# Kernel optimization log

Hardware: AMD Instinct MI355X
Metric: run time of the kernel (lower is better)

## Reference

```python
import jax, jax.numpy as jnp
import numpy as np

B, S, D, E, H, K = 2, 2048, 1024, 8, 2048, 2
EM_ITERS = 5
LB_WEIGHT = 0.1
EPS = 1e-8


def setup_inputs() -> dict:
    key = jax.random.key(0)
    ks = jax.random.split(key, 12)
    sc = 0.02
    return {
        "x": jax.random.normal(ks[0], (B, S, D), jnp.float32),
        "gate_W": jax.random.normal(ks[1], (D, E), jnp.float32) * sc,
        "gate_b": jnp.zeros((E,), jnp.float32),
        "gate_temp": jnp.ones((1,), jnp.float32),
        "W1": jax.random.normal(ks[2], (E, D, H), jnp.float32) * sc,
        "b1": jnp.zeros((E, H), jnp.float32),
        "W2": jax.random.normal(ks[3], (E, H, D), jnp.float32) * sc,
        "b2": jnp.zeros((E, D), jnp.float32),
        "sW1": jax.random.normal(ks[4], (D, H), jnp.float32) * sc,
        "sb1": jnp.zeros((H,), jnp.float32),
        "sW2": jax.random.normal(ks[5], (H, D), jnp.float32) * sc,
        "sb2": jnp.zeros((D,), jnp.float32),
    }


def reference(x, gate_W, gate_b, gate_temp, W1, b1, W2, b2, sW1, sb1, sW2, sb2):
    Bq, Sq, Dq = x.shape
    T = Bq * Sq
    xf = x.reshape(T, Dq)  # (T, D)

    # Router: gate linear + learned temperature
    gate_logits = xf @ gate_W + gate_b              # (T, E)
    tempered = gate_logits / gate_temp               # (T, E)
    expert_weights = jax.nn.softmax(tempered, axis=-1)
    _, topk_idx = jax.lax.top_k(expert_weights, K)   # (T, K) int32
    first = topk_idx[:, 0]

    # Load-balance loss: KL(uniform || empirical top-1 usage) (fresh counters)
    usage = jnp.zeros((E,), jnp.float32).at[first].add(1.0)
    actual = usage / jnp.float32(T)
    actual = actual + EPS
    actual = actual / actual.sum()
    u = jnp.float32(1.0 / E)
    kl = jnp.sum(u * (jnp.log(u) - jnp.log(actual)))
    load_balance_loss = LB_WEIGHT * kl

    # EM expert-load reweighting on tempered logits
    scores = jax.nn.softmax(tempered, axis=-1)       # (T, E)
    p = jnp.full((E,), 1.0 / E, jnp.float32)
    for _ in range(EM_ITERS):
        ea = scores * p                               # (T, E)
        ea = ea / (ea.sum(axis=-1, keepdims=True) + EPS)
        counts = ea.sum(axis=0)                       # (E,)
        p = counts / (counts.sum() + EPS)
    balanced = scores * p                             # (T, E)

    # All-expert FFN (dense, equivalent to per-expert masked compute)
    h = jax.nn.relu(jnp.einsum('td,edh->teh', xf, W1) + b1)  # (T, E, H)
    eo = jnp.einsum('teh,ehd->ted', h, W2) + b2              # (T, E, D)

    # Combine top-k experts with balanced weights
    w_k = jnp.take_along_axis(balanced, topk_idx, axis=1)        # (T, K)
    out_k = jnp.take_along_axis(eo, topk_idx[:, :, None], axis=1)  # (T, K, D)
    out = jnp.einsum('tk,tkd->td', w_k, out_k)                   # (T, D)

    # Shared expert, weighted by 0.1
    shared = jax.nn.relu(xf @ sW1 + sb1) @ sW2 + sb2
    out = out + 0.1 * shared

    return out.reshape(Bq, Sq, Dq), load_balance_loss
```

## Files before the change

### kernel.cpp

```cpp
#include <hip/hip_runtime.h>
#include <math.h>

#define T_TOK 4096
#define D_DIM 1024
#define H_DIM 2048
#define NE 8
#define EPSF 1e-8f
#define G1_GEMM 896
#define G2_GEMM 448
#define NTR128 1152

typedef __attribute__((ext_vector_type(8))) short bf16x8;
typedef __attribute__((ext_vector_type(4))) float f32x4;

__device__ __forceinline__ unsigned short f2bf(float f) {
  unsigned u = __float_as_uint(f);
  u += 0x7fffu + ((u >> 16) & 1u);
  return (unsigned short)(u >> 16);
}

__device__ __forceinline__ void gload_lds16(const void* g, void* l) {
  __builtin_amdgcn_global_load_lds(
      (const __attribute__((address_space(1))) unsigned int*)g,
      (__attribute__((address_space(3))) unsigned int*)l, 16, 0, 0);
}

#define WAITV(n) asm volatile("s_waitcnt vmcnt(" #n ")" ::: "memory")
#define BARR()                                  \
  do {                                          \
    asm volatile("" ::: "memory");              \
    __builtin_amdgcn_s_barrier();               \
    asm volatile("" ::: "memory");              \
  } while (0)

__device__ __forceinline__ void transpose_tile128(const float* __restrict__ src,
                                                  unsigned short* __restrict__ dst,
                                                  int R, int C, int r0, int c0, int tid,
                                                  float* tile) {
#pragma unroll
  for (int k = 0; k < 8; ++k) {
    int id = tid + k * 512;
    int row = id >> 5, c4 = (id & 31) * 4;
    float4 v = *(const float4*)(src + (size_t)(r0 + row) * C + c0 + c4);
    float* tr = tile + row * 129 + c4;
    tr[0] = v.x; tr[1] = v.y; tr[2] = v.z; tr[3] = v.w;
  }
  __syncthreads();
#pragma unroll
  for (int k = 0; k < 4; ++k) {
    int id = tid + k * 512;
    int oc = id >> 4;
    int rbase = (id & 15) * 8;
    uint4 wv;
    unsigned* wp = (unsigned*)&wv;
#pragma unroll
    for (int j = 0; j < 4; ++j) {
      unsigned lo = f2bf(tile[(rbase + 2 * j) * 129 + oc]);
      unsigned hi = f2bf(tile[(rbase + 2 * j + 1) * 129 + oc]);
      wp[j] = lo | (hi << 16);
    }
    *(uint4*)(dst + (size_t)(c0 + oc) * R + r0 + rbase) = wv;
  }
}

__global__ __launch_bounds__(512, 4) void prep2_kernel(
    const float* __restrict__ x, const float* __restrict__ gW, const float* __restrict__ gb,
    const float* __restrict__ gtemp, const float* __restrict__ W1, const float* __restrict__ sW1,
    unsigned short* __restrict__ W1t, unsigned short* __restrict__ sW1t,
    unsigned short* __restrict__ xb, float* __restrict__ scores, int* __restrict__ idx,
    unsigned* __restrict__ usage, unsigned* __restrict__ cnt, int* __restrict__ perm) {
  __shared__ char psm[67584];
  int b = blockIdx.x, tid = threadIdx.x;
  if (b >= 512) {
    int l = b - 512;
    int m = l >> 7, rem = l & 127;
    int c0 = (rem & 15) * 128, r0 = (rem >> 4) * 128;
    const float* src = (m < NE) ? W1 + (size_t)m * D_DIM * H_DIM : sW1;
    unsigned short* dst = (m < NE) ? W1t + (size_t)m * D_DIM * H_DIM : sW1t;
    transpose_tile128(src, dst, D_DIM, H_DIM, r0, c0, tid, (float*)psm);
    return;
  }
  float* gWl = (float*)psm;
  int* toks = (int*)(psm + 36864);
  int wave = tid >> 6, lane = tid & 63;
  int t0 = b * 8;
#pragma unroll
  for (int k = 0; k < 4; ++k) {
    int q = tid + k * 512;
    float4 f = ((const float4*)gW)[q];
    int d = q >> 1, eo = (q & 1) * 4;
    float* dstv = &gWl[d * 9 + eo];
    dstv[0] = f.x; dstv[1] = f.y; dstv[2] = f.z; dstv[3] = f.w;
  }
  __syncthreads();
  int t = t0 + wave;
  const float* xr = x + (size_t)t * D_DIM;
  unsigned short* xbr = xb + (size_t)t * D_DIM;
  float part[NE];
#pragma unroll
  for (int e = 0; e < NE; ++e) part[e] = 0.f;
#pragma unroll
  for (int i = 0; i < 16; ++i) {
    int d = lane + 64 * i;
    float xv = xr[d];
    xbr[d] = f2bf(xv);
    const float* g = &gWl[d * 9];
#pragma unroll
    for (int e = 0; e < NE; ++e) part[e] += xv * g[e];
  }
#pragma unroll
  for (int e = 0; e < NE; ++e) {
    float v = part[e];
    for (int off = 32; off; off >>= 1) v += __shfl_xor(v, off);
    part[e] = v;
  }
  float temp = gtemp[0];
  float mx = -1e30f;
#pragma unroll
  for (int e = 0; e < NE; ++e) { part[e] = (part[e] + gb[e]) / temp; mx = fmaxf(mx, part[e]); }
  float s = 0.f;
#pragma unroll
  for (int e = 0; e < NE; ++e) { part[e] = expf(part[e] - mx); s += part[e]; }
  float inv = 1.0f / s;
#pragma unroll
  for (int e = 0; e < NE; ++e) part[e] *= inv;
  if (lane == 0) {
    float4* sp = (float4*)(scores + (size_t)t * NE);
    sp[0] = make_float4(part[0], part[1], part[2], part[3]);
    sp[1] = make_float4(part[4], part[5], part[6], part[7]);
    int i0 = 0; float b0 = part[0];
#pragma unroll
    for (int e = 1; e < NE; ++e) if (part[e] > b0) { b0 = part[e]; i0 = e; }
    int i1 = -1; float b1 = -1e30f;
#pragma unroll
    for (int e = 0; e < NE; ++e) if (e != i0 && part[e] > b1) { b1 = part[e]; i1 = e; }
    idx[t * 2] = i0; idx[t * 2 + 1] = i1;
    toks[wave * 2] = i0; toks[wave * 2 + 1] = i1;
  }
  __syncthreads();
  if (tid < NE) {
    int c0 = 0, c1 = 0;
#pragma unroll
    for (int j = 0; j < 8; ++j) {
      if (toks[j * 2] == tid) ++c0;
      if (toks[j * 2 + 1] == tid) ++c1;
    }
    if (c0) atomicAdd(&usage[tid], (unsigned)c0);
    int tot = c0 + c1;
    if (tot) {
      unsigned bb = atomicAdd(&cnt[tid], (unsigned)tot);
      int p = 0;
#pragma unroll
      for (int j = 0; j < 8; ++j) {
        if (toks[j * 2] == tid) perm[(size_t)tid * T_TOK + bb + p++] = (t0 + j) * 2;
        if (toks[j * 2 + 1] == tid) perm[(size_t)tid * T_TOK + bb + p++] = (t0 + j) * 2 + 1;
      }
    }
  }
}

__device__ __forceinline__ void em_block512(const float* __restrict__ scores,
                                            const unsigned* __restrict__ usage,
                                            float* __restrict__ p_out, float* __restrict__ loss_out,
                                            int tid, char* smem) {
  float* p_sh = (float*)smem;
  float* cw = p_sh + 8;
  float* counts_sh = cw + 64;
  int wave = tid >> 6, lane = tid & 63;
  float s[8][NE];
#pragma unroll
  for (int rr = 0; rr < 8; ++rr) {
    int row = tid + rr * 512;
    const float4* sp = (const float4*)(scores + (size_t)row * NE);
    float4 a = sp[0], b = sp[1];
    s[rr][0] = a.x; s[rr][1] = a.y; s[rr][2] = a.z; s[rr][3] = a.w;
    s[rr][4] = b.x; s[rr][5] = b.y; s[rr][6] = b.z; s[rr][7] = b.w;
  }
  if (tid < NE) p_sh[tid] = 1.0f / NE;
  __syncthreads();
  for (int it = 0; it < 5; ++it) {
    float p[NE];
#pragma unroll
    for (int e = 0; e < NE; ++e) p[e] = p_sh[e];
    float c[NE];
#pragma unroll
    for (int e = 0; e < NE; ++e) c[e] = 0.f;
#pragma unroll
    for (int rr = 0; rr < 8; ++rr) {
      float denom = 0.f;
#pragma unroll
      for (int e = 0; e < NE; ++e) denom += s[rr][e] * p[e];
      float inv = 1.0f / (denom + EPSF);
#pragma unroll
      for (int e = 0; e < NE; ++e) c[e] += s[rr][e] * p[e] * inv;
    }
#pragma unroll
    for (int e = 0; e < NE; ++e) {
      float v = c[e];
      for (int off = 32; off; off >>= 1) v += __shfl_xor(v, off);
      c[e] = v;
    }
    if (lane == 0) {
#pragma unroll
      for (int e = 0; e < NE; ++e) cw[wave * 8 + e] = c[e];
    }
    __syncthreads();
    if (tid < NE) {
      float tot = 0.f;
#pragma unroll
      for (int w = 0; w < 8; ++w) tot += cw[w * 8 + tid];
      counts_sh[tid] = tot;
    }
    __syncthreads();
    if (tid < NE) {
      float total = 0.f;
#pragma unroll
      for (int e = 0; e < NE; ++e) total += counts_sh[e];
      p_sh[tid] = counts_sh[tid] / (total + EPSF);
    }
    __syncthreads();
  }
  if (tid < NE) p_out[tid] = p_sh[tid];
  if (tid == 0) {
    float actual[NE]; float norm = 0.f;
#pragma unroll
    for (int e = 0; e < NE; ++e) { actual[e] = (float)usage[e] / (float)T_TOK + EPSF; norm += actual[e]; }
    float u = 1.0f / NE;
    float kl = 0.f;
#pragma unroll
    for (int e = 0; e < NE; ++e) kl += u * (logf(u) - logf(actual[e] / norm));
    loss_out[0] = 0.1f * kl;
  }
}

template <int KDIM, int NDIM, bool RELU, bool MODE1>
__device__ __forceinline__ void gemm_body(
    unsigned short* lds, int flat,
    const unsigned short* __restrict__ A, const unsigned short* __restrict__ WE,
    const unsigned short* __restrict__ WS, const float* __restrict__ biasE,
    const float* __restrict__ biasS, const int* __restrict__ perm,
    const unsigned* __restrict__ cnt, void* __restrict__ outp) {
  constexpr int BM = 256, BN = 128, BK = 32;
  constexpr int NT = NDIM / BN;
  constexpr int NKT = KDIM / BK;

  int tc[9];
#pragma unroll
  for (int i = 0; i < NE; ++i) tc[i] = ((int)cnt[i] + 255) >> 8;
  tc[8] = T_TOK / 256;
  int nt = 0;
#pragma unroll
  for (int i = 0; i < 9; ++i) nt += tc[i];
  int W = nt * NT;
  int xcd = flat & 7, pos = flat >> 3;
  int q = W >> 3, r = W & 7;
  int mycount = q + (xcd < r ? 1 : 0);
  if (pos >= mycount) return;
  int mystart = xcd * q + (xcd < r ? xcd : r);
  int w = mystart + pos;
  int ti = w / NT;
  int n0 = (w % NT) * BN;
  int e = 0, mt = ti;
  while (mt >= tc[e]) { mt -= tc[e]; ++e; }
  int m0 = mt * BM;
  int cnt_e = (e == NE) ? T_TOK : (int)cnt[e];

  const unsigned short* Bmat = (e == NE) ? WS : WE + (size_t)e * KDIM * NDIM;
  const float* bias = (e == NE) ? biasS : biasE + (size_t)e * NDIM;

  int tid = threadIdx.x, wave = tid >> 6, lane = tid & 63;
  int wm = wave >> 1, wn = wave & 1;
  int frow = lane & 15, fks = lane >> 4;

  auto garf = [&](int rrow) {
    int ar = m0 + rrow; if (ar > cnt_e - 1) ar = cnt_e - 1;
    int gar;
    if (e == NE) gar = MODE1 ? ar : (2 * T_TOK + ar);
    else { int v = perm[(size_t)e * T_TOK + ar]; gar = MODE1 ? (v >> 1) : v; }
    return gar;
  };
  int r0a = wave * 16 + (lane >> 2);
  int r1a = 128 + wave * 16 + (lane >> 2);
  int rb = wave * 16 + (lane >> 2);
  int g0 = (r0a & 3) ^ ((r0a >> 2) & 3);
  int g1 = (r1a & 3) ^ ((r1a >> 2) & 3);
  int gbv = (rb & 3) ^ ((rb >> 2) & 3);
  const unsigned short* aptr0 = A + (size_t)garf(r0a) * KDIM + (((lane & 3) ^ g0) << 3);
  const unsigned short* aptr1 = A + (size_t)garf(r1a) * KDIM + (((lane & 3) ^ g1) << 3);
  const unsigned short* bptr = Bmat + (size_t)(n0 + rb) * KDIM + (((lane & 3) ^ gbv) << 3);

  auto stA = [&](int t, int ab) {
    gload_lds16(aptr0 + t * BK, &lds[ab * 8192 + wave * 512]);
    gload_lds16(aptr1 + t * BK, &lds[ab * 8192 + 4096 + wave * 512]);
  };
  auto stB = [&](int t) {
    gload_lds16(bptr + t * BK, &lds[24576 + (t & 1) * 4096 + wave * 512]);
  };

  auto rdA = [&](int ab, int m) -> bf16x8 {
    int rr = wm * 64 + m * 16 + frow;
    int sp = fks ^ ((rr & 3) ^ ((rr >> 2) & 3));
    return *(const bf16x8*)&lds[ab * 8192 + rr * 32 + sp * 8];
  };
  auto rdB = [&](int bb, int j) -> bf16x8 {
    int rr = wn * 64 + j * 16 + frow;
    int sp = fks ^ ((rr & 3) ^ ((rr >> 2) & 3));
    return *(const bf16x8*)&lds[24576 + bb * 4096 + rr * 32 + sp * 8];
  };

  f32x4 acc[4][4];
#pragma unroll
  for (int m = 0; m < 4; ++m)
#pragma unroll
    for (int j = 0; j < 4; ++j) acc[m][j] = (f32x4){0.f, 0.f, 0.f, 0.f};

  stA(0, 0); stB(0); stA(1, 1);
  WAITV(2);
  BARR();

  int ab = 0;
  for (int t = 0; t < NKT; ++t) {
    int bb = t & 1;
    bf16x8 a[4], b[4];
#pragma unroll
    for (int m = 0; m < 4; ++m) a[m] = rdA(ab, m);
#pragma unroll
    for (int j = 0; j < 4; ++j) b[j] = rdB(bb, j);
    if (t + 1 < NKT) stB(t + 1);
    if (t + 2 < NKT) { int ab2 = ab + 2; if (ab2 >= 3) ab2 -= 3; stA(t + 2, ab2); }
    BARR();
    __builtin_amdgcn_s_setprio(1);
#pragma unroll
    for (int m = 0; m < 4; ++m)
#pragma unroll
      for (int j = 0; j < 4; ++j)
        acc[m][j] = __builtin_amdgcn_mfma_f32_16x16x32_bf16(a[m], b[j], acc[m][j], 0, 0, 0);
    __builtin_amdgcn_s_setprio(0);
    if (t + 1 < NKT) {
      if (t + 2 < NKT) { WAITV(2); } else { WAITV(0); }
      BARR();
    }
    ab = (ab == 2) ? 0 : ab + 1;
  }

#pragma unroll
  for (int m = 0; m < 4; ++m) {
#pragma unroll
    for (int qq = 0; qq < 4; ++qq) {
      int rt = wm * 64 + m * 16 + (lane >> 4) * 4 + qq;
      if (m0 + rt >= cnt_e) continue;
      int rr;
      if (e == NE) rr = 2 * T_TOK + m0 + rt;
      else rr = perm[(size_t)e * T_TOK + m0 + rt];
#pragma unroll
      for (int j = 0; j < 4; ++j) {
        int col = n0 + wn * 64 + j * 16 + (lane & 15);
        float val = acc[m][j][qq] + bias[col];
        if (RELU) val = fmaxf(val, 0.f);
        if (MODE1)
          ((unsigned short*)outp)[(size_t)rr * NDIM + col] = f2bf(val);
        else
          ((float*)outp)[(size_t)rr * NDIM + col] = val;
      }
    }
  }
}

__global__ __launch_bounds__(512, 4) void gemm1_kernel(
    const unsigned short* __restrict__ xb, const unsigned short* __restrict__ W1t,
    const unsigned short* __restrict__ sW1t, const float* __restrict__ b1,
    const float* __restrict__ sb1, const int* __restrict__ perm, const unsigned* __restrict__ cnt,
    unsigned short* __restrict__ Hbuf,
    const float* __restrict__ W2, const float* __restrict__ sW2,
    unsigned short* __restrict__ W2t, unsigned short* __restrict__ sW2t,
    const float* __restrict__ scores, const unsigned* __restrict__ usage,
    float* __restrict__ pbuf, float* __restrict__ loss_out) {
  __shared__ char smem[67584];
  int flat = blockIdx.x;
  if (flat < G1_GEMM) {
    gemm_body<D_DIM, H_DIM, true, true>((unsigned short*)smem, flat, xb, W1t, sW1t, b1, sb1,
                                        perm, cnt, (void*)Hbuf);
    return;
  }
  int l = flat - G1_GEMM;
  if (l < NTR128) {
    int m = l >> 7, rem = l & 127;
    int c0 = (rem & 7) * 128, r0 = (rem >> 3) * 128;
    const float* src = (m < NE) ? W2 + (size_t)m * H_DIM * D_DIM : sW2;
    unsigned short* dst = (m < NE) ? W2t + (size_t)m * H_DIM * D_DIM : sW2t;
    transpose_tile128(src, dst, H_DIM, D_DIM, r0, c0, threadIdx.x, (float*)smem);
    return;
  }
  em_block512(scores, usage, pbuf, loss_out, threadIdx.x, smem);
}

template <int KDIM, int NDIM, bool RELU, bool MODE1>
__global__ __launch_bounds__(512, 4) void gemm_kernel(
    const unsigned short* __restrict__ A, const unsigned short* __restrict__ WE,
    const unsigned short* __restrict__ WS, const float* __restrict__ biasE,
    const float* __restrict__ biasS, const int* __restrict__ perm,
    const unsigned* __restrict__ cnt, void* __restrict__ outp) {
  __shared__ char smem[67584];
  gemm_body<KDIM, NDIM, RELU, MODE1>((unsigned short*)smem, blockIdx.x, A, WE, WS, biasE, biasS,
                                     perm, cnt, outp);
}

__global__ void combine_kernel(const float* __restrict__ ebuf, const float* __restrict__ scores,
                               const float* __restrict__ p, const int* __restrict__ idx,
                               float* __restrict__ out) {
  int gid = blockIdx.x * blockDim.x + threadIdx.x;
  int t = gid >> 8;
  int d4 = gid & 255;
  int e0 = idx[t * 2], e1 = idx[t * 2 + 1];
  float w0 = scores[(size_t)t * NE + e0] * p[e0];
  float w1 = scores[(size_t)t * NE + e1] * p[e1];
  const float4* r0 = (const float4*)(ebuf + (size_t)(t * 2) * D_DIM);
  const float4* r1 = (const float4*)(ebuf + (size_t)(t * 2 + 1) * D_DIM);
  const float4* rs = (const float4*)(ebuf + (size_t)(2 * T_TOK + t) * D_DIM);
  float4 a = r0[d4], b = r1[d4], c = rs[d4];
  float4 o;
  o.x = w0 * a.x + w1 * b.x + 0.1f * c.x;
  o.y = w0 * a.y + w1 * b.y + 0.1f * c.y;
  o.z = w0 * a.z + w1 * b.z + 0.1f * c.z;
  o.w = w0 * a.w + w1 * b.w + 0.1f * c.w;
  ((float4*)out)[gid] = o;
}

extern "C" void kernel_launch(void* const* d_in, const int* in_sizes, int n_in,
                              void* d_out, int out_size, void* d_ws, size_t ws_size,
                              hipStream_t stream) {
  const float* x     = (const float*)d_in[0];
  const float* gW    = (const float*)d_in[1];
  const float* gb    = (const float*)d_in[2];
  const float* gtemp = (const float*)d_in[3];
  const float* W1    = (const float*)d_in[4];
  const float* b1    = (const float*)d_in[5];
  const float* W2    = (const float*)d_in[6];
  const float* b2    = (const float*)d_in[7];
  const float* sW1   = (const float*)d_in[8];
  const float* sb1   = (const float*)d_in[9];
  const float* sW2   = (const float*)d_in[10];
  const float* sb2   = (const float*)d_in[11];
  float* out = (float*)d_out;

  char* ws = (char*)d_ws;
  size_t off = 0;
  auto take = [&](size_t b) { char* ptr = ws + off; off += (b + 255) & ~(size_t)255; return ptr; };
  unsigned short* xb   = (unsigned short*)take((size_t)T_TOK * D_DIM * 2);
  unsigned short* W1t  = (unsigned short*)take((size_t)NE * H_DIM * D_DIM * 2);
  unsigned short* sW1t = (unsigned short*)take((size_t)H_DIM * D_DIM * 2);
  unsigned short* W2t  = (unsigned short*)take((size_t)NE * D_DIM * H_DIM * 2);
  unsigned short* sW2t = (unsigned short*)take((size_t)D_DIM * H_DIM * 2);
  unsigned short* Hbuf = (unsigned short*)take((size_t)3 * T_TOK * H_DIM * 2);
  float* ebuf          = (float*)take((size_t)3 * T_TOK * D_DIM * 4);
  float* scores        = (float*)take((size_t)T_TOK * NE * 4);
  int* idx             = (int*)take((size_t)T_TOK * 2 * 4);
  int* perm            = (int*)take((size_t)NE * T_TOK * 4);
  unsigned* cnt        = (unsigned*)take(256);
  unsigned* usage      = (unsigned*)take(256);
  float* pbuf          = (float*)take(256);
  (void)n_in; (void)in_sizes; (void)out_size; (void)ws_size;

  hipMemsetAsync(cnt, 0, 512, stream);
  prep2_kernel<<<512 + NTR128, 512, 0, stream>>>(x, gW, gb, gtemp, W1, sW1, W1t, sW1t, xb,
                                                 scores, idx, usage, cnt, perm);
  gemm1_kernel<<<G1_GEMM + NTR128 + 1, 512, 0, stream>>>(
      xb, W1t, sW1t, b1, sb1, perm, cnt, Hbuf, W2, sW2, W2t, sW2t, scores, usage, pbuf,
      out + (size_t)T_TOK * D_DIM);
  gemm_kernel<H_DIM, D_DIM, false, false><<<G2_GEMM, 512, 0, stream>>>(
      Hbuf, W2t, sW2t, b2, sb2, perm, cnt, (void*)ebuf);
  combine_kernel<<<(T_TOK * D_DIM / 4) / 256, 256, 0, stream>>>(ebuf, scores, pbuf, idx, out);
}
```

Measured before the change: 203.5 us.

## Retile grouped GEMM to 128x256x64 with triple-buffered B and larger LDS

Changes the grouped expert GEMM tile from 256x128 with BK=32 to 128x256 with BK=64. A is now double-buffered and B triple-buffered, using a new XOR swizzle on 64-element rows, and each iteration issues two MFMA k-steps. LDS grows to 128KB, so launch bounds drop to one block per CU. The grid sizes are recomputed for the new tile counts. The aim is fewer barriers per unit of work and better reuse of the per-expert weight tiles. In exchange, occupancy drops and padding waste on small per-expert token counts rises with the finer M granularity.

```diff
diff --git a/kernel.cpp b/kernel.cpp
--- a/kernel.cpp
+++ b/kernel.cpp
@@ -6,8 +6,8 @@
 #define H_DIM 2048
 #define NE 8
 #define EPSF 1e-8f
-#define G1_GEMM 896
-#define G2_GEMM 448
+#define G1_GEMM 832
+#define G2_GEMM 416
 #define NTR128 1152
 
 typedef __attribute__((ext_vector_type(8))) short bf16x8;
@@ -26,6 +26,7 @@
 }
 
 #define WAITV(n) asm volatile("s_waitcnt vmcnt(" #n ")" ::: "memory")
+#define WAITL() asm volatile("s_waitcnt lgkmcnt(0)" ::: "memory")
 #define BARR()                                  \
   do {                                          \
     asm volatile("" ::: "memory");              \
@@ -240,14 +241,14 @@
     const unsigned short* __restrict__ WS, const float* __restrict__ biasE,
     const float* __restrict__ biasS, const int* __restrict__ perm,
     const unsigned* __restrict__ cnt, void* __restrict__ outp) {
-  constexpr int BM = 256, BN = 128, BK = 32;
+  constexpr int BM = 128, BN = 256, BK = 64;
   constexpr int NT = NDIM / BN;
   constexpr int NKT = KDIM / BK;
 
   int tc[9];
 #pragma unroll
-  for (int i = 0; i < NE; ++i) tc[i] = ((int)cnt[i] + 255) >> 8;
-  tc[8] = T_TOK / 256;
+  for (int i = 0; i < NE; ++i) tc[i] = ((int)cnt[i] + 127) >> 7;
+  tc[8] = T_TOK / 128;
   int nt = 0;
 #pragma unroll
   for (int i = 0; i < 9; ++i) nt += tc[i];
@@ -269,43 +270,50 @@
   const float* bias = (e == NE) ? biasS : biasE + (size_t)e * NDIM;
 
   int tid = threadIdx.x, wave = tid >> 6, lane = tid & 63;
-  int wm = wave >> 1, wn = wave & 1;
+  int wm = wave >> 2, wn = wave & 3;
   int frow = lane & 15, fks = lane >> 4;
-
-  auto garf = [&](int rrow) {
-    int ar = m0 + rrow; if (ar > cnt_e - 1) ar = cnt_e - 1;
+  int sr = tid >> 3, slot = tid & 7;
+
+  const unsigned short* aptr[2];
+#pragma unroll
+  for (int h = 0; h < 2; ++h) {
+    int rloc = h * 64 + sr;
+    int ar = m0 + rloc;
+    if (ar > cnt_e - 1) ar = cnt_e - 1;
     int gar;
     if (e == NE) gar = MODE1 ? ar : (2 * T_TOK + ar);
     else { int v = perm[(size_t)e * T_TOK + ar]; gar = MODE1 ? (v >> 1) : v; }
-    return gar;
-  };
-  int r0a = wave * 16 + (lane >> 2);
-  int r1a = 128 + wave * 16 + (lane >> 2);
-  int rb = wave * 16 + (lane >> 2);
-  int g0 = (r0a & 3) ^ ((r0a >> 2) & 3);
-  int g1 = (r1a & 3) ^ ((r1a >> 2) & 3);
-  int gbv = (rb & 3) ^ ((rb >> 2) & 3);
-  const unsigned short* aptr0 = A + (size_t)garf(r0a) * KDIM + (((lane & 3) ^ g0) << 3);
-  const unsigned short* aptr1 = A + (size_t)garf(r1a) * KDIM + (((lane & 3) ^ g1) << 3);
-  const unsigned short* bptr = Bmat + (size_t)(n0 + rb) * KDIM + (((lane & 3) ^ gbv) << 3);
-
-  auto stA = [&](int t, int ab) {
-    gload_lds16(aptr0 + t * BK, &lds[ab * 8192 + wave * 512]);
-    gload_lds16(aptr1 + t * BK, &lds[ab * 8192 + 4096 + wave * 512]);
+    aptr[h] = A + (size_t)gar * KDIM + ((slot ^ (rloc & 7)) << 3);
+  }
+  const unsigned short* bptr[4];
+#pragma unroll
+  for (int qq = 0; qq < 4; ++qq) {
+    int rb = qq * 64 + sr;
+    bptr[qq] = Bmat + (size_t)(n0 + rb) * KDIM + ((slot ^ (rb & 7)) << 3);
+  }
+
+  auto stA = [&](int t) {
+    int d = (t & 1) * 8192;
+    gload_lds16(aptr[0] + t * BK, &lds[d + tid * 8]);
+    gload_lds16(aptr[1] + t * BK, &lds[d + 4096 + tid * 8]);
   };
   auto stB = [&](int t) {
-    gload_lds16(bptr + t * BK, &lds[24576 + (t & 1) * 4096 + wave * 512]);
+    int d = 16384 + (t % 3) * 16384;
+    gload_lds16(bptr[0] + t * BK, &lds[d + tid * 8]);
+    gload_lds16(bptr[1] + t * BK, &lds[d + 4096 + tid * 8]);
+    gload_lds16(bptr[2] + t * BK, &lds[d + 8192 + tid * 8]);
+    gload_lds16(bptr[3] + t * BK, &lds[d + 12288 + tid * 8]);
   };
 
-  auto rdA = [&](int ab, int m) -> bf16x8 {
+  auto rdA = [&](int ab, int ks, int m) -> bf16x8 {
     int rr = wm * 64 + m * 16 + frow;
-    int sp = fks ^ ((rr & 3) ^ ((rr >> 2) & 3));
-    return *(const bf16x8*)&lds[ab * 8192 + rr * 32 + sp * 8];
+    int s2 = (ks * 4 + fks) ^ (rr & 7);
+    return *(const bf16x8*)&lds[ab * 8192 + rr * 64 + s2 * 8];
   };
-  auto rdB = [&](int bb, int j) -> bf16x8 {
+  auto rdB = [&](int bb, int ks, int j) -> bf16x8 {
     int rr = wn * 64 + j * 16 + frow;
-    int sp = fks ^ ((rr & 3) ^ ((rr >> 2) & 3));
-    return *(const bf16x8*)&lds[24576 + bb * 4096 + rr * 32 + sp * 8];
+    int s2 = (ks * 4 + fks) ^ (rr & 7);
+    return *(const bf16x8*)&lds[16384 + bb * 16384 + rr * 64 + s2 * 8];
   };
 
   f32x4 acc[4][4];
@@ -314,33 +322,36 @@
 #pragma unroll
     for (int j = 0; j < 4; ++j) acc[m][j] = (f32x4){0.f, 0.f, 0.f, 0.f};
 
-  stA(0, 0); stB(0); stA(1, 1);
-  WAITV(2);
+  stA(0); stB(0); stA(1); stB(1);
+  WAITV(6);
   BARR();
 
-  int ab = 0;
   for (int t = 0; t < NKT; ++t) {
-    int bb = t & 1;
-    bf16x8 a[4], b[4];
-#pragma unroll
-    for (int m = 0; m < 4; ++m) a[m] = rdA(ab, m);
-#pragma unroll
-    for (int j = 0; j < 4; ++j) b[j] = rdB(bb, j);
-    if (t + 1 < NKT) stB(t + 1);
-    if (t + 2 < NKT) { int ab2 = ab + 2; if (ab2 >= 3) ab2 -= 3; stA(t + 2, ab2); }
+    int ab = t & 1, bb = t % 3;
+    bf16x8 a0[4], a1[4], b0[4], b1[4];
+#pragma unroll
+    for (int m = 0; m < 4; ++m) { a0[m] = rdA(ab, 0, m); a1[m] = rdA(ab, 1, m); }
+#pragma unroll
+    for (int j = 0; j < 4; ++j) { b0[j] = rdB(bb, 0, j); b1[j] = rdB(bb, 1, j); }
+    WAITL();
     BARR();
+    if (t + 2 < NKT) { stA(t + 2); stB(t + 2); }
     __builtin_amdgcn_s_setprio(1);
 #pragma unroll
     for (int m = 0; m < 4; ++m)
 #pragma unroll
       for (int j = 0; j < 4; ++j)
-        acc[m][j] = __builtin_amdgcn_mfma_f32_16x16x32_bf16(a[m], b[j], acc[m][j], 0, 0, 0);
+        acc[m][j] = __builtin_amdgcn_mfma_f32_16x16x32_bf16(a0[m], b0[j], acc[m][j], 0, 0, 0);
+#pragma unroll
+    for (int m = 0; m < 4; ++m)
+#pragma unroll
+      for (int j = 0; j < 4; ++j)
+        acc[m][j] = __builtin_amdgcn_mfma_f32_16x16x32_bf16(a1[m], b1[j], acc[m][j], 0, 0, 0);
     __builtin_amdgcn_s_setprio(0);
     if (t + 1 < NKT) {
-      if (t + 2 < NKT) { WAITV(2); } else { WAITV(0); }
+      if (t + 2 < NKT) { WAITV(6); } else { WAITV(0); }
       BARR();
     }
-    ab = (ab == 2) ? 0 : ab + 1;
   }
 
 #pragma unroll
@@ -366,7 +377,7 @@
   }
 }
 
-__global__ __launch_bounds__(512, 4) void gemm1_kernel(
+__global__ __launch_bounds__(512, 1) void gemm1_kernel(
     const unsigned short* __restrict__ xb, const unsigned short* __restrict__ W1t,
     const unsigned short* __restrict__ sW1t, const float* __restrict__ b1,
     const float* __restrict__ sb1, const int* __restrict__ perm, const unsigned* __restrict__ cnt,
@@ -375,7 +386,7 @@
     unsigned short* __restrict__ W2t, unsigned short* __restrict__ sW2t,
     const float* __restrict__ scores, const unsigned* __restrict__ usage,
     float* __restrict__ pbuf, float* __restrict__ loss_out) {
-  __shared__ char smem[67584];
+  __shared__ char smem[131072];
   int flat = blockIdx.x;
   if (flat < G1_GEMM) {
     gemm_body<D_DIM, H_DIM, true, true>((unsigned short*)smem, flat, xb, W1t, sW1t, b1, sb1,
@@ -395,12 +406,12 @@
 }
 
 template <int KDIM, int NDIM, bool RELU, bool MODE1>
-__global__ __launch_bounds__(512, 4) void gemm_kernel(
+__global__ __launch_bounds__(512, 1) void gemm_kernel(
     const unsigned short* __restrict__ A, const unsigned short* __restrict__ WE,
     const unsigned short* __restrict__ WS, const float* __restrict__ biasE,
     const float* __restrict__ biasS, const int* __restrict__ perm,
     const unsigned* __restrict__ cnt, void* __restrict__ outp) {
-  __shared__ char smem[67584];
+  __shared__ char smem[131072];
   gemm_body<KDIM, NDIM, RELU, MODE1>((unsigned short*)smem, blockIdx.x, A, WE, WS, biasE, biasS,
                                      perm, cnt, outp);
 }
```

Measured after the change: 223.1 us. 1.1x slower.
